# Kernel tuning notes

Measured on AMD Instinct MI355X. Metric: run time of the kernel, lower is better.

## Reference

```python
import jax, jax.numpy as jnp
from jax import lax
import numpy as np

CH = 512      # ch_in = c_in = c_out
P = 8         # p: channels per group
NG = CH // P  # depthwise groups
PG = CH // P  # pointwise groups
EPS = 1e-5
DN = ('NCHW', 'OIHW', 'NCHW')


def leaky(x):
    return jnp.where(x >= 0, x, 0.01 * x)  # LeakyReLU default slope


def setup_inputs() -> dict:
    key = jax.random.key(0)
    ks = jax.random.split(key, 8)
    N, H, W = 16, 64, 64
    return {
        'style_encoding': jax.random.normal(ks[0], (N, 512, 4, 4), jnp.float32),
        'content_in': jax.random.normal(ks[1], (N, CH, H, W), jnp.float32),
        'dw_w': jax.random.normal(ks[2], (P, 512, 2, 2), jnp.float32) * 0.05,
        'dw_b': jax.random.normal(ks[3], (P,), jnp.float32) * 0.05,
        'pk_w': jax.random.normal(ks[4], (P, 512), jnp.float32) * 0.05,
        'pk_b': jax.random.normal(ks[5], (P,), jnp.float32) * 0.05,
        'pb_w': jax.random.normal(ks[6], (CH, 512), jnp.float32) * 0.05,
        'pb_b': jax.random.normal(ks[7], (CH,), jnp.float32) * 0.05,
    }


def reference(style_encoding, content_in, dw_w, dw_b, pk_w, pk_b, pb_w, pb_b):
    N, _, H, W = content_in.shape
    # --- KernelPredictor ---
    # depthwise kernels: 2x2 valid conv on 4x4 style map -> [N, P, 3, 3]
    d = lax.conv_general_dilated(style_encoding, dw_w, (1, 1), 'VALID',
                                 dimension_numbers=DN)
    d = leaky(d + dw_b[None, :, None, None])  # [N, P, 3, 3]
    # expand: same [P,3,3] filter for every output channel -> [N, CH, P, 3, 3]
    depthwise = jnp.broadcast_to(d[:, None], (N, CH, P, 3, 3))
    # avg-pool 4 on 4x4 style map == global mean -> [N, 512]
    s_d = jnp.mean(style_encoding, axis=(2, 3))
    pk = jnp.einsum('nc,oc->no', s_d, pk_w) + pk_b       # [N, P]  (1x1 conv)
    bias = jnp.einsum('nc,oc->no', s_d, pb_w) + pb_b     # [N, CH] (1x1 conv)

    # --- per-sample grouped convs, batched by folding batch into groups ---
    padded = jnp.pad(content_in, ((0, 0), (0, 0), (1, 1), (1, 1)), mode='reflect')
    xr = padded.reshape(1, N * CH, H + 2, W + 2)
    wr = depthwise.reshape(N * CH, P, 3, 3)
    depth = lax.conv_general_dilated(xr, wr, (1, 1), 'VALID',
                                     feature_group_count=N * NG,
                                     dimension_numbers=DN)
    depth = depth.reshape(N, CH, H, W)

    # pointwise 1x1 grouped conv: weight [N, CH, P, 1, 1], identical over out
    # channels within a sample (expand); groups = PG, CH//PG == P out ch/group
    depth_g = depth.reshape(N, PG, P, H, W)
    pw_g = jnp.broadcast_to(pk[:, None, None, :], (N, PG, P, P))  # [n,g,o,j]
    out = jnp.einsum('ngjhw,ngoj->ngohw', depth_g, pw_g).reshape(N, CH, H, W)
    predicted = leaky(out + bias[:, :, None, None])

    # --- instance-norm of content (AdaIN calc_mean_std, unbiased var) ---
    mean = jnp.mean(content_in, axis=(2, 3), keepdims=True)
    std = jnp.sqrt(jnp.var(content_in, axis=(2, 3), keepdims=True, ddof=1) + EPS)
    normalized = (content_in - mean) / std
    return normalized * predicted
```

## Files before the change

kernel.cpp:

```cpp
#include <hip/hip_runtime.h>
#include <math.h>

#define PLANE 4096
#define EPS 1e-5f

typedef float f4 __attribute__((ext_vector_type(4)));

__device__ __forceinline__ float leaky(float x) { return x >= 0.f ? x : 0.01f * x; }

__device__ __forceinline__ float wave_sum(float v) {
    #pragma unroll
    for (int off = 32; off; off >>= 1) v += __shfl_xor(v, off, 64);
    return v;
}

__global__ __launch_bounds__(256) void prep_kernel(
    const float* __restrict__ style,
    const float* __restrict__ content,
    const float* __restrict__ dw_w,
    const float* __restrict__ dw_b,
    const float* __restrict__ pk_w,
    const float* __restrict__ pk_b,
    float* __restrict__ sd_out,
    float* __restrict__ S_out,
    float* __restrict__ d_pred,
    float* __restrict__ mean_out,
    float* __restrict__ rstd_out)
{
    const int blk = blockIdx.x;
    const int t = threadIdx.x;
    const int wave = t >> 6, lane = t & 63;

    __shared__ float ls[4], lq[4];
    __shared__ float s_sd[512];
    __shared__ float red[4];

    if (blk < 8192) {
        const float4* base = (const float4*)(content + (size_t)blk * PLANE);
        float s = 0.f, q = 0.f;
        #pragma unroll
        for (int k = 0; k < 4; ++k) {
            float4 v = base[k * 256 + t];
            s += v.x + v.y + v.z + v.w;
            q += v.x * v.x + v.y * v.y + v.z * v.z + v.w * v.w;
        }
        #pragma unroll
        for (int off = 32; off; off >>= 1) {
            s += __shfl_xor(s, off, 64);
            q += __shfl_xor(q, off, 64);
        }
        if (lane == 0) { ls[wave] = s; lq[wave] = q; }
        __syncthreads();
        if (t == 0) {
            float S = ls[0] + ls[1] + ls[2] + ls[3];
            float Q = lq[0] + lq[1] + lq[2] + lq[3];
            float m = S * (1.f / 4096.f);
            float var = (Q - 4096.f * m * m) * (1.f / 4095.f);
            mean_out[blk] = m;
            rstd_out[blk] = rsqrtf(var + EPS);
        }
    } else if (blk < 8208) {
        const int n = blk - 8192;
        const float* sb = style + (size_t)n * 8192;
        #pragma unroll
        for (int qd = 0; qd < 2; ++qd) {
            int c = t + 256 * qd;
            const float4* sp = (const float4*)sb + c * 4;
            float4 a = sp[0], b = sp[1], d = sp[2], e = sp[3];
            float s = a.x + a.y + a.z + a.w + b.x + b.y + b.z + b.w
                    + d.x + d.y + d.z + d.w + e.x + e.y + e.z + e.w;
            s *= (1.f / 16.f);
            s_sd[c] = s;
            sd_out[n * 512 + c] = s;
        }
        __syncthreads();
        float part = 0.f;
        #pragma unroll
        for (int o = 0; o < 8; ++o)
            part += pk_w[o * 512 + t] * s_sd[t]
                  + pk_w[o * 512 + t + 256] * s_sd[t + 256];
        part = wave_sum(part);
        if (lane == 0) red[wave] = part;
        __syncthreads();
        if (t == 0) {
            float S = red[0] + red[1] + red[2] + red[3];
            #pragma unroll
            for (int o = 0; o < 8; ++o) S += pk_b[o];
            S_out[n] = S;
        }
    } else {
        const int n = blk - 8208;
        const float* sb = style + (size_t)n * 8192;
        const float4* wp = (const float4*)dw_w;
        for (int rr = 0; rr < 18; ++rr) {
            int r = wave * 18 + rr;
            int j = r / 9, pos = r % 9, y = pos / 3, x = pos % 3;
            float acc = 0.f;
            #pragma unroll
            for (int i = 0; i < 8; ++i) {
                int c = lane + 64 * i;
                float4 w = wp[j * 512 + c];
                const float* s = sb + c * 16 + y * 4 + x;
                acc += s[0] * w.x + s[1] * w.y + s[4] * w.z + s[5] * w.w;
            }
            acc = wave_sum(acc);
            if (lane == 0) d_pred[n * 72 + r] = leaky(acc + dw_b[j]);
        }
    }
}

__global__ __launch_bounds__(256, 3) void main_kernel(
    const float* __restrict__ content,
    const float* __restrict__ d_pred,
    const float* __restrict__ S_in,
    const float* __restrict__ sd,
    const float* __restrict__ pb_w,
    const float* __restrict__ pb_b,
    const float* __restrict__ mean_in,
    const float* __restrict__ rstd_in,
    float* __restrict__ out)
{
    const int b    = blockIdx.x;
    const int tile = b & 3;
    const int g    = (b >> 2) & 63;
    const int n    = b >> 8;
    const int t  = threadIdx.x;
    const int tx = t & 15, ty = t >> 4;
    const int h  = tile * 16 + ty;
    const int x0 = tx * 4;

    __shared__ float s_d[72];
    __shared__ float s_S;
    __shared__ float s_bias[8], s_mean[8], s_rstd[8];

    if (t < 72) s_d[t] = d_pred[n * 72 + t];
    if (t == 80) s_S = S_in[n];
    if (t >= 96 && t < 104) {
        int o = t - 96;
        int c = n * 512 + g * 8 + o;
        s_mean[o] = mean_in[c];
        s_rstd[o] = rstd_in[c];
    }
    {
        const int o = t >> 5, l = t & 31;
        const float* pw  = pb_w + (size_t)(g * 8 + o) * 512;
        const float* sdn = sd + n * 512;
        float acc = 0.f;
        #pragma unroll
        for (int i = 0; i < 16; ++i) acc += pw[l + 32 * i] * sdn[l + 32 * i];
        #pragma unroll
        for (int off = 16; off; off >>= 1) acc += __shfl_xor(acc, off, 64);
        if (l == 0) s_bias[o] = acc + pb_b[g * 8 + o];
    }
    __syncthreads();

    const float* cbase = content + (size_t)(n * 512 + g * 8) * PLANE;
    float D0 = 0.f, D1 = 0.f, D2 = 0.f, D3 = 0.f;

    #pragma unroll
    for (int j = 0; j < 8; ++j) {
        const float* cj = cbase + j * PLANE;
        #pragma unroll
        for (int r = 0; r < 3; ++r) {
            int y = h - 1 + r;
            int ry = y < 0 ? 1 : (y > 63 ? 62 : y);
            float4 v = *(const float4*)(cj + ry * 64 + x0);
            float lv = __shfl_up(v.w, 1, 64);
            float rv = __shfl_down(v.x, 1, 64);
            float xm = (tx == 0)  ? v.y : lv;
            float xp = (tx == 15) ? v.z : rv;
            const float w0 = s_d[j * 9 + r * 3 + 0];
            const float w1 = s_d[j * 9 + r * 3 + 1];
            const float w2 = s_d[j * 9 + r * 3 + 2];
            D0 += w0 * xm  + w1 * v.x + w2 * v.y;
            D1 += w0 * v.x + w1 * v.y + w2 * v.z;
            D2 += w0 * v.y + w1 * v.z + w2 * v.w;
            D3 += w0 * v.z + w1 * v.w + w2 * xp;
        }
    }

    const float S = s_S;
    const float P0 = D0 * S, P1 = D1 * S, P2 = D2 * S, P3 = D3 * S;
    float* obase = out + (size_t)(n * 512 + g * 8) * PLANE + h * 64 + x0;
    #pragma unroll
    for (int o = 0; o < 8; ++o) {
        float4 v = *(const float4*)(cbase + o * PLANE + h * 64 + x0);
        float bb = s_bias[o], m = s_mean[o], rs = s_rstd[o];
        f4 res;
        res.x = (v.x - m) * rs * leaky(P0 + bb);
        res.y = (v.y - m) * rs * leaky(P1 + bb);
        res.z = (v.z - m) * rs * leaky(P2 + bb);
        res.w = (v.w - m) * rs * leaky(P3 + bb);
        __builtin_nontemporal_store(res, (f4*)(obase + o * PLANE));
    }
}

extern "C" void kernel_launch(void* const* d_in, const int* in_sizes, int n_in,
                              void* d_out, int out_size, void* d_ws, size_t ws_size,
                              hipStream_t stream) {
    const float* style   = (const float*)d_in[0];
    const float* content = (const float*)d_in[1];
    const float* dw_w    = (const float*)d_in[2];
    const float* dw_b    = (const float*)d_in[3];
    const float* pk_w    = (const float*)d_in[4];
    const float* pk_b    = (const float*)d_in[5];
    const float* pb_w    = (const float*)d_in[6];
    const float* pb_b    = (const float*)d_in[7];
    float* out = (float*)d_out;
    float* ws  = (float*)d_ws;

    const int N = 16;
    float* sd_ws   = ws;
    float* d_pred  = sd_ws + N * 512;
    float* S_ws    = d_pred + N * 72;
    float* mean_ws = S_ws + N;
    float* rstd_ws = mean_ws + N * 512;

    prep_kernel<<<8224, 256, 0, stream>>>(style, content, dw_w, dw_b, pk_w, pk_b,
                                          sd_ws, S_ws, d_pred, mean_ws, rstd_ws);
    main_kernel<<<N * 64 * 4, 256, 0, stream>>>(content, d_pred, S_ws, sd_ws,
                                                pb_w, pb_b, mean_ws, rstd_ws, out);
}
```

Measured before the change: 292.3 us.

## Stage content tile with halo rows in LDS for depthwise conv reuse

The main kernel now loads each block's 8-channel, 18-row haloed tile into shared memory once and reads every stencil row and the normalization input from LDS. This replaces the repeated global loads of overlapping rows and the cross-lane shuffles. It also drops the occupancy hint in launch bounds and switches the output from nontemporal stores to ordinary stores. The roughly 39KB of LDS per block limits how many blocks fit on a CU, and ordinary stores may pollute the cache.

```diff
diff --git a/kernel.cpp b/kernel.cpp
--- a/kernel.cpp
+++ b/kernel.cpp
@@ -3,6 +3,10 @@
 
 #define PLANE 4096
 #define EPS 1e-5f
+
+#define ROWS 18
+#define LDW  68
+#define LPLANE (ROWS * LDW)
 
 typedef float f4 __attribute__((ext_vector_type(4)));
 
@@ -109,7 +113,7 @@
     }
 }
 
-__global__ __launch_bounds__(256, 3) void main_kernel(
+__global__ __launch_bounds__(256) void main_kernel(
     const float* __restrict__ content,
     const float* __restrict__ d_pred,
     const float* __restrict__ S_in,
@@ -129,6 +133,7 @@
     const int h  = tile * 16 + ty;
     const int x0 = tx * 4;
 
+    __shared__ float s_x[8 * LPLANE];
     __shared__ float s_d[72];
     __shared__ float s_S;
     __shared__ float s_bias[8], s_mean[8], s_rstd[8];
@@ -152,23 +157,34 @@
         for (int off = 16; off; off >>= 1) acc += __shfl_xor(acc, off, 64);
         if (l == 0) s_bias[o] = acc + pb_b[g * 8 + o];
     }
+
+    const float* cbase = content + (size_t)(n * 512 + g * 8) * PLANE;
+    #pragma unroll
+    for (int i = 0; i < 9; ++i) {
+        int q   = t + 256 * i;
+        int p   = q / 288;
+        int rem = q - p * 288;
+        int row = rem >> 4;
+        int c4  = rem & 15;
+        int y   = tile * 16 + row - 1;
+        int ry  = y < 0 ? 1 : (y > 63 ? 62 : y);
+        float4 v = *(const float4*)(cbase + p * PLANE + ry * 64 + c4 * 4);
+        *(f4*)(s_x + p * LPLANE + row * LDW + c4 * 4) = { v.x, v.y, v.z, v.w };
+    }
     __syncthreads();
 
-    const float* cbase = content + (size_t)(n * 512 + g * 8) * PLANE;
+    const int xmi = (tx == 0)  ? 1  : x0 - 1;
+    const int xpi = (tx == 15) ? 62 : x0 + 4;
     float D0 = 0.f, D1 = 0.f, D2 = 0.f, D3 = 0.f;
-
     #pragma unroll
     for (int j = 0; j < 8; ++j) {
-        const float* cj = cbase + j * PLANE;
+        const float* base = s_x + j * LPLANE;
         #pragma unroll
         for (int r = 0; r < 3; ++r) {
-            int y = h - 1 + r;
-            int ry = y < 0 ? 1 : (y > 63 ? 62 : y);
-            float4 v = *(const float4*)(cj + ry * 64 + x0);
-            float lv = __shfl_up(v.w, 1, 64);
-            float rv = __shfl_down(v.x, 1, 64);
-            float xm = (tx == 0)  ? v.y : lv;
-            float xp = (tx == 15) ? v.z : rv;
+            const float* rowp = base + (ty + r) * LDW;
+            f4 v = *(const f4*)(rowp + x0);
+            float xm = rowp[xmi];
+            float xp = rowp[xpi];
             const float w0 = s_d[j * 9 + r * 3 + 0];
             const float w1 = s_d[j * 9 + r * 3 + 1];
             const float w2 = s_d[j * 9 + r * 3 + 2];
@@ -184,14 +200,14 @@
     float* obase = out + (size_t)(n * 512 + g * 8) * PLANE + h * 64 + x0;
     #pragma unroll
     for (int o = 0; o < 8; ++o) {
-        float4 v = *(const float4*)(cbase + o * PLANE + h * 64 + x0);
+        f4 v = *(const f4*)(s_x + o * LPLANE + (ty + 1) * LDW + x0);
         float bb = s_bias[o], m = s_mean[o], rs = s_rstd[o];
-        f4 res;
+        float4 res;
         res.x = (v.x - m) * rs * leaky(P0 + bb);
         res.y = (v.y - m) * rs * leaky(P1 + bb);
         res.z = (v.z - m) * rs * leaky(P2 + bb);
         res.w = (v.w - m) * rs * leaky(P3 + bb);
-        __builtin_nontemporal_store(res, (f4*)(obase + o * PLANE));
+        *(float4*)(obase + o * PLANE) = res;
     }
 }
 
```

Result: no change. 292.8 us (+0.2%).
